# Kernel tuning notes

Hardware: AMD Instinct MI355X
Metric: run time of the kernel (lower is better)

## Reference

```python
import jax, jax.numpy as jnp
import numpy as np
import math

N_NODES = 10000
N_EDGES = 30000
N_FEAT = 128
N_GRAPHS = 50
HEADS = 8
OUT_DIM = 10


def _lin_params(key, fin, fout):
    kw, kb = jax.random.split(key)
    s = 1.0 / math.sqrt(fin)
    w = jax.random.uniform(kw, (fin, fout), jnp.float32, -s, s)
    b = jax.random.uniform(kb, (fout,), jnp.float32, -s, s)
    return w, b


def setup_inputs() -> dict:
    key = jax.random.key(0)
    ks = jax.random.split(key, 20)
    inp = {}
    inp["x"] = jax.random.normal(ks[0], (N_NODES, N_FEAT), jnp.float32)
    inp["edge_index"] = jax.random.randint(ks[1], (2, N_EDGES), 0, N_NODES)
    inp["batch"] = jnp.sort(jax.random.randint(ks[2], (N_NODES,), 0, N_GRAPHS))
    # (fin, out_channels) per layer; internal width = out_channels * HEADS
    dims = [(128, 512), (512, 256), (256, 64)]
    ki = 3
    for i, (fin, cout) in enumerate(dims, 1):
        hc = cout * HEADS
        inp[f"q{i}_w"], inp[f"q{i}_b"] = _lin_params(ks[ki], fin, hc); ki += 1
        inp[f"k{i}_w"], inp[f"k{i}_b"] = _lin_params(ks[ki], fin, hc); ki += 1
        inp[f"v{i}_w"], inp[f"v{i}_b"] = _lin_params(ks[ki], fin, hc); ki += 1
        inp[f"s{i}_w"], inp[f"s{i}_b"] = _lin_params(ks[ki], fin, cout); ki += 1
    inp["gate_w"], inp["gate_b"] = _lin_params(ks[ki], 64, 1); ki += 1
    inp["fc_w"], inp["fc_b"] = _lin_params(ks[ki], 64, OUT_DIM)
    return inp


def _tconv(x, src, dst, qw, qb, kw_, kb_, vw, vb, sw, sb):
    # PyG TransformerConv, heads=HEADS, concat=False (mean over heads), root_weight=True
    N = x.shape[0]
    hc = qw.shape[1]
    C = hc // HEADS
    q = (x @ qw + qb).reshape(N, HEADS, C)
    k = (x @ kw_ + kb_).reshape(N, HEADS, C)
    v = (x @ vw + vb).reshape(N, HEADS, C)
    # per-edge attention logits [E, H]
    alpha = (q[dst] * k[src]).sum(-1) * (1.0 / math.sqrt(C))
    # segment softmax over incoming edges of each destination node
    m = jax.ops.segment_max(alpha, dst, num_segments=N)
    ex = jnp.exp(alpha - m[dst])
    den = jax.ops.segment_sum(ex, dst, num_segments=N)
    w = ex / jnp.maximum(den[dst], 1e-16)
    agg = jax.ops.segment_sum(w[:, :, None] * v[src], dst, num_segments=N)  # [N,H,C]
    return agg.mean(axis=1) + x @ sw + sb


def reference(x, edge_index, batch,
              q1_w, q1_b, k1_w, k1_b, v1_w, v1_b, s1_w, s1_b,
              q2_w, q2_b, k2_w, k2_b, v2_w, v2_b, s2_w, s2_b,
              q3_w, q3_b, k3_w, k3_b, v3_w, v3_b, s3_w, s3_b,
              gate_w, gate_b, fc_w, fc_b):
    src, dst = edge_index[0], edge_index[1]
    h = jax.nn.elu(_tconv(x, src, dst, q1_w, q1_b, k1_w, k1_b, v1_w, v1_b, s1_w, s1_b))
    h = jax.nn.elu(_tconv(h, src, dst, q2_w, q2_b, k2_w, k2_b, v2_w, v2_b, s2_w, s2_b))
    h = jax.nn.elu(_tconv(h, src, dst, q3_w, q3_b, k3_w, k3_b, v3_w, v3_b, s3_w, s3_b))
    # GlobalAttention pooling: softmax(gate) within each graph, weighted sum
    gate = h @ gate_w + gate_b  # [N,1]
    gm = jax.ops.segment_max(gate, batch, num_segments=N_GRAPHS)
    ge = jnp.exp(gate - gm[batch])
    gd = jax.ops.segment_sum(ge, batch, num_segments=N_GRAPHS)
    g = ge / jnp.maximum(gd[batch], 1e-16)
    pooled = jax.ops.segment_sum(g * h, batch, num_segments=N_GRAPHS)  # [G,64]
    return pooled @ fc_w + fc_b
```

## Files before the change

kernel.cpp:

```cpp
#include <hip/hip_runtime.h>
#include <stdint.h>
#include <math.h>

#define NN 10000
#define NE 30000
#define NG 50
#define NH 8

typedef _Float16 f16;
typedef _Float16 f16x2 __attribute__((ext_vector_type(2)));
typedef _Float16 f16x4 __attribute__((ext_vector_type(4)));
typedef _Float16 f16x8 __attribute__((ext_vector_type(8)));
typedef float f32x4 __attribute__((ext_vector_type(4)));

__device__ inline void async16(f16* l, const f16* g) {
    __builtin_amdgcn_global_load_lds((const __attribute__((address_space(1))) void*)g,
                                     (__attribute__((address_space(3))) void*)l, 16, 0, 0);
}

__global__ void hist_kernel(const int* __restrict__ dst, int* __restrict__ deg, int E) {
    int e = blockIdx.x * blockDim.x + threadIdx.x;
    if (e < E) atomicAdd(&deg[dst[e]], 1);
}

__global__ __launch_bounds__(1024) void scan_goffs(const int* __restrict__ deg, int* __restrict__ offs,
                                                   int* __restrict__ cursor,
                                                   const int* __restrict__ batch, int* __restrict__ goffs) {
    if (blockIdx.x == 1) {
        int g = threadIdx.x;
        if (g > NG) return;
        int lo = 0, hi = NN;
        while (lo < hi) {
            int mid = (lo + hi) >> 1;
            if (batch[mid] < g) lo = mid + 1; else hi = mid;
        }
        goffs[g] = lo;
        return;
    }
    __shared__ int tot[1024];
    const int t = threadIdx.x;
    const int base = t * 10;
    int v[10];
    int s = 0;
#pragma unroll
    for (int i = 0; i < 10; ++i) {
        int idx = base + i;
        v[i] = (idx < NN) ? deg[idx] : 0;
        s += v[i];
    }
    tot[t] = s;
    __syncthreads();
    for (int d2 = 1; d2 < 1024; d2 <<= 1) {
        int add = (t >= d2) ? tot[t - d2] : 0;
        __syncthreads();
        tot[t] += add;
        __syncthreads();
    }
    int run = tot[t] - s;
    if (t == 0) offs[0] = 0;
#pragma unroll
    for (int i = 0; i < 10; ++i) {
        int idx = base + i;
        if (idx < NN) cursor[idx] = run;
        run += v[i];
        if (idx < NN) offs[idx + 1] = run;
    }
}

__global__ void scatter_kernel(const int* __restrict__ src, const int* __restrict__ dst,
                               int* __restrict__ cursor, int* __restrict__ srcCSR, int E) {
    int e = blockIdx.x * blockDim.x + threadIdx.x;
    if (e < E) {
        int p = atomicAdd(&cursor[dst[e]], 1);
        srcCSR[p] = src[e];
    }
}

__global__ void sort_csr(const int* __restrict__ offs, int* __restrict__ srcCSR) {
    int n = blockIdx.x * blockDim.x + threadIdx.x;
    if (n >= NN) return;
    int s = offs[n], e = offs[n + 1];
    for (int i = s + 1; i < e; ++i) {
        int v = srcCSR[i];
        int j = i - 1;
        while (j >= s && srcCSR[j] > v) { srcCSR[j + 1] = srcCSR[j]; --j; }
        srcCSR[j + 1] = v;
    }
}

__global__ void cvt3_kernel(const float* __restrict__ a, f16* __restrict__ ao, int na,
                            const float* __restrict__ b, f16* __restrict__ bo, int nb2,
                            const float* __restrict__ c, f16* __restrict__ co, int nc) {
    int i = blockIdx.x * blockDim.x + threadIdx.x;
    if (i < na) ao[i] = (f16)a[i];
    else if (i < na + nb2) { int j = i - na; bo[j] = (f16)b[j]; }
    else if (i < na + nb2 + nc) { int j = i - na - nb2; co[j] = (f16)c[j]; }
}

__global__ __launch_bounds__(256) void prep4t2(
        const float* W0a, int n0a, const float* W1a, int n1a,
        const float* W2a, int n2a, const float* W3a, int n3a,
        const float* b0a, const float* b1a, const float* b2a, const float* b3a,
        f16* Bta, float* biasa, int Ka, int Na,
        const float* W0b, int n0b, const float* W1b, int n1b,
        const float* W2b, int n2b, const float* W3b, int n3b,
        const float* b0b, const float* b1b, const float* b2b, const float* b3b,
        f16* Btb, float* biasb, int Kb, int Nb) {
    const int z = blockIdx.z;
    const float *W0 = z ? W0b : W0a, *W1 = z ? W1b : W1a, *W2 = z ? W2b : W2a, *W3 = z ? W3b : W3a;
    const float *b0 = z ? b0b : b0a, *b1 = z ? b1b : b1a, *b2 = z ? b2b : b2a, *b3 = z ? b3b : b3a;
    const int n0 = z ? n0b : n0a, n1 = z ? n1b : n1a, n2 = z ? n2b : n2a, n3 = z ? n3b : n3a;
    const int K = z ? Kb : Ka, Ntot = z ? Nb : Na;
    f16* Bt = z ? Btb : Bta;
    float* bias = z ? biasb : biasa;
    if ((int)blockIdx.x * 64 >= K || (int)blockIdx.y * 64 >= Ntot) return;

    __shared__ float tile[64][65];
    const int k0 = blockIdx.x * 64;
    const int nb = blockIdx.y * 64;
    const int tid = threadIdx.x;
    const int tn = tid & 63;
    const int t4 = tid >> 6;
#pragma unroll
    for (int i = 0; i < 16; ++i) {
        int kl = t4 + i * 4;
        int k = k0 + kl;
        int n = nb + tn;
        float w = 0.0f;
        int m = n;
        if (m < n0) w = W0[(size_t)k * n0 + m];
        else { m -= n0;
            if (m < n1) w = W1[(size_t)k * n1 + m];
            else { m -= n1;
                if (m < n2) w = W2[(size_t)k * n2 + m];
                else { m -= n2; if (m < n3) w = W3[(size_t)k * n3 + m]; }
            }
        }
        tile[kl][tn] = w;
    }
    if (blockIdx.x == 0 && t4 == 0) {
        int n = nb + tn;
        float bv = 0.0f;
        int m = n;
        if (m < n0) bv = b0[m];
        else { m -= n0;
            if (m < n1) bv = b1[m];
            else { m -= n1;
                if (m < n2) bv = b2[m];
                else { m -= n2; if (m < n3) bv = b3[m]; }
            }
        }
        bias[n] = bv;
    }
    __syncthreads();
#pragma unroll
    for (int i = 0; i < 16; ++i) {
        int nl = t4 + i * 4;
        Bt[(size_t)(nb + nl) * K + k0 + tn] = (f16)tile[tn][nl];
    }
}

__global__ __launch_bounds__(256) void prepU(const float* __restrict__ qw, const float* __restrict__ qb,
                                             const float* __restrict__ kw, const float* __restrict__ kb,
                                             f16* __restrict__ BtY, float* __restrict__ biasY,
                                             int fin, int hc, int C) {
    const int wid = blockIdx.x * 4 + ((int)threadIdx.x >> 6);
    const int lane = threadIdx.x & 63;
    if (wid >= fin * 16) return;
    const int k = wid >> 4;
    const int idx = wid & 15;
    const int h = idx & 7, isV = idx >> 3;
    const float* W = isV ? kw : qw;
    const float* bvec = isV ? qb : kb;
    float s = 0.0f;
    for (int c = lane; c < C; c += 64) s += W[(size_t)k * hc + h * C + c] * bvec[h * C + c];
#pragma unroll
    for (int o = 32; o > 0; o >>= 1) s += __shfl_down(s, o, 64);
    if (lane == 0) BtY[(size_t)(8 * fin + isV * 8 + h) * fin + k] = (f16)s;
    if (wid < 8) {
        float cc = 0.0f;
        for (int c = lane; c < C; c += 64) cc += qb[wid * C + c] * kb[wid * C + c];
#pragma unroll
        for (int o = 32; o > 0; o >>= 1) cc += __shfl_down(cc, o, 64);
        if (lane == 0) biasY[8 * fin + wid] = cc;
    }
}

__global__ __launch_bounds__(256) void prepZB(const float* __restrict__ vw, const float* __restrict__ sw,
                                              const float* __restrict__ vb, const float* __restrict__ sb,
                                              f16* __restrict__ Bt2, float* __restrict__ biasZ) {
    __shared__ f16 tile[32][65];
    const int k0 = blockIdx.x * 32, c0 = blockIdx.y * 64;
    const int tid = threadIdx.x;
#pragma unroll
    for (int i = 0; i < 8; ++i) {
        int idx = tid + i * 256;
        int kl = idx >> 6, cl = idx & 63;
        int k = k0 + kl, c = c0 + cl;
        float v = 0.0f;
        if (k < 1024)      v = vw[(size_t)(k & 127) * 4096 + (k >> 7) * 512 + c];
        else if (k < 1152) v = sw[(size_t)(k - 1024) * 512 + c];
        else if (k < 1160) v = vb[(k - 1152) * 512 + c];
        tile[kl][cl] = (f16)v;
    }
    if (blockIdx.x == 0 && tid < 64) biasZ[c0 + tid] = sb[c0 + tid];
    __syncthreads();
    const int cl = tid >> 2, kl = (tid & 3) * 8;
    f16x8 v;
#pragma unroll
    for (int t = 0; t < 8; ++t) v[t] = tile[kl + t][cl];
    *(f16x8*)(Bt2 + (size_t)(c0 + cl) * 1184 + k0 + kl) = v;
}

__global__ __launch_bounds__(256) void gemm128(const f16* __restrict__ A, int lda, int zA,
                                               const f16* __restrict__ Bt, int ldb, int zB,
                                               const float* __restrict__ bias,
                                               f16* __restrict__ C, int ldc, int zC,
                                               float* __restrict__ Sf,
                                               int M, int Np, int K, int hcS, int Sw, int act) {
    __shared__ f16 smem[24576];
    const int rm = blockIdx.x * 128;
    if (rm >= M) return;
    A  += (size_t)blockIdx.z * zA;
    Bt += (size_t)blockIdx.z * zB;
    C  += (size_t)blockIdx.z * zC;
    const int tid  = threadIdx.x;
    const int lane = tid & 63;
    const int wave = tid >> 6;
    const int l16  = lane & 15;
    const int quad = lane >> 4;
    const int cn   = blockIdx.y * 128;
    const int wrow = (wave >> 1) * 64;
    const int wcol = (wave & 1) * 64;

    const int rS  = tid >> 2;
    const int kc  = ((tid & 3) ^ ((tid >> 3) & 3)) << 3;
    int rowA0 = rm + rS;       if (rowA0 >= M) rowA0 = M - 1;
    int rowA1 = rm + rS + 64;  if (rowA1 >= M) rowA1 = M - 1;
    const f16* gA0 = A + (size_t)rowA0 * lda + kc;
    const f16* gA1 = A + (size_t)rowA1 * lda + kc;
    const f16* gB0 = Bt + (size_t)(cn + rS) * ldb + kc;
    const f16* gB1 = Bt + (size_t)(cn + rS + 64) * ldb + kc;

    const int swf = (l16 >> 1) & 3;
    const int rdAoff = (wrow + l16) * 32 + ((quad ^ swf) << 3);
    const int rdBoff = 4096 + (wcol + l16) * 32 + ((quad ^ swf) << 3);

    f32x4 acc[4][4] = {};

    auto stage_load = [&](int slot) {
        f16* base = smem + slot * 8192;
        async16(base + tid * 8, gA0);
        async16(base + tid * 8 + 2048, gA1);
        async16(base + 4096 + tid * 8, gB0);
        async16(base + 4096 + tid * 8 + 2048, gB1);
        gA0 += 32; gA1 += 32; gB0 += 32; gB1 += 32;
    };

    const int NI = K >> 5;
    stage_load(0);
    stage_load(1);

    int slot = 0;
    for (int i = 0; i < NI; ++i) {
        if (i + 1 < NI) asm volatile("s_waitcnt vmcnt(4)" ::: "memory");
        else            asm volatile("s_waitcnt vmcnt(0)" ::: "memory");
        asm volatile("s_barrier" ::: "memory");
        if (i + 2 < NI) {
            int s2 = slot + 2; if (s2 >= 3) s2 -= 3;
            stage_load(s2);
        }
        const f16* sb = smem + slot * 8192;
        f16x8 av[4], bv[4];
#pragma unroll
        for (int ii = 0; ii < 4; ++ii) av[ii] = *(const f16x8*)(sb + rdAoff + ii * 512);
#pragma unroll
        for (int j = 0; j < 4; ++j) bv[j] = *(const f16x8*)(sb + rdBoff + j * 512);
#pragma unroll
        for (int ii = 0; ii < 4; ++ii)
#pragma unroll
            for (int j = 0; j < 4; ++j)
                acc[ii][j] = __builtin_amdgcn_mfma_f32_16x16x32_f16(bv[j], av[ii], acc[ii][j], 0, 0, 0);
        ++slot; if (slot == 3) slot = 0;
    }
    __syncthreads();

    f16* sC = smem;
    for (int round = 0; round < 2; ++round) {
        if ((wave >> 1) == round) {
#pragma unroll
            for (int j = 0; j < 4; ++j) {
                const int cb = wcol + j * 16 + quad * 4;
                const float4 bb = *(const float4*)(bias + cn + cb);
#pragma unroll
                for (int i = 0; i < 4; ++i) {
                    const int r = i * 16 + l16;
                    float v0 = acc[i][j][0] + bb.x;
                    float v1 = acc[i][j][1] + bb.y;
                    float v2 = acc[i][j][2] + bb.z;
                    float v3 = acc[i][j][3] + bb.w;
                    if (act) {
                        v0 = v0 > 0.0f ? v0 : (__expf(v0) - 1.0f);
                        v1 = v1 > 0.0f ? v1 : (__expf(v1) - 1.0f);
                        v2 = v2 > 0.0f ? v2 : (__expf(v2) - 1.0f);
                        v3 = v3 > 0.0f ? v3 : (__expf(v3) - 1.0f);
                    }
                    f16x4 o;
                    o[0] = (f16)v0; o[1] = (f16)v1; o[2] = (f16)v2; o[3] = (f16)v3;
                    *(f16x4*)(sC + r * 136 + cb) = o;
                    if (Sf) {
                        const int sc = cn + cb - hcS;
                        if (sc >= 0 && sc < Sw) {
                            const int grow = rm + round * 64 + r;
                            if (grow < M) {
                                float4 sv = { v0, v1, v2, v3 };
                                *(float4*)(Sf + (size_t)grow * Sw + sc) = sv;
                            }
                        }
                    }
                }
            }
        }
        __syncthreads();
#pragma unroll
        for (int it = 0; it < 4; ++it) {
            const int r = it * 16 + (tid >> 4);
            const int ch = tid & 15;
            const int grow = rm + round * 64 + r;
            if (grow < M) {
                f16x8 v = *(const f16x8*)(sC + r * 136 + ch * 8);
                *(f16x8*)(C + (size_t)grow * ldc + cn + ch * 8) = v;
            }
        }
        __syncthreads();
    }
}

__global__ __launch_bounds__(256) void alpha_zagg(const f16* __restrict__ Y, const f16* __restrict__ X,
                                                  const int* __restrict__ offs,
                                                  const int* __restrict__ srcCSR,
                                                  f16* __restrict__ Z,
                                                  int strideY, float scale) {
    const int fin = 128;
    const int n = blockIdx.x;
    const int e0 = offs[n];
    int d = offs[n + 1] - e0;
    if (d > 256) d = 256;

    __shared__ __align__(16) f16 sy[1024];
    __shared__ float sew[256 * NH];
    __shared__ float sv[256 * NH];
    __shared__ int sed[256];
    __shared__ float su[NH];
    __shared__ __align__(16) f16 sx[32 * 128];
    const int tid = threadIdx.x;

    const f16* Yn = Y + (size_t)n * strideY;
    for (int c = tid; c < fin; c += 256) ((f16x8*)sy)[c] = ((const f16x8*)Yn)[c];
    if (tid < NH) su[tid] = (float)Yn[8 * fin + tid];
    for (int e = tid; e < d; e += 256) {
        int s = srcCSR[e0 + e];
        sed[e] = s;
        f16x8 vv = *(const f16x8*)(Y + (size_t)s * strideY + 8 * fin + 8);
#pragma unroll
        for (int t = 0; t < 8; ++t) sv[e * NH + t] = (float)vv[t];
    }
    __syncthreads();

    {
        const int wv = tid >> 6, lane = tid & 63;
        for (int e = wv; e < d; e += 4) {
            const f16x8* kg = (const f16x8*)(X + (size_t)sed[e] * fin);
#pragma unroll
            for (int p = 0; p < 2; ++p) {
                const int ci = p * 64 + lane;
                const int head = ci >> 4;
                const int kcn = ci & 15;
                f16x8 yv = ((const f16x8*)sy)[ci];
                f16x8 xv = kg[kcn];
                float acc = 0.0f;
#pragma unroll
                for (int t = 0; t < 8; ++t) acc += (float)yv[t] * (float)xv[t];
#pragma unroll
                for (int o = 8; o > 0; o >>= 1) acc += __shfl_down(acc, o, 16);
                if ((lane & 15) == 0)
                    sew[e * NH + head] = (acc + su[head] + sv[e * NH + head]) * scale;
            }
        }
    }
    __syncthreads();

    if (tid < NH) {
        const int h = tid;
        float m = -3.0e38f;
        for (int e = 0; e < d; ++e) m = fmaxf(m, sew[e * NH + h]);
        float den = 0.0f;
        for (int e = 0; e < d; ++e) {
            float ex = __expf(sew[e * NH + h] - m);
            sew[e * NH + h] = ex;
            den += ex;
        }
        float inv = 1.0f / (fmaxf(den, 1e-16f) * (float)NH);
        for (int e = 0; e < d; ++e) sew[e * NH + h] *= inv;
    }
    __syncthreads();

    const int h = tid >> 5;
    const int f0 = (tid * 4) & 127;
    float a0 = 0.0f, a1 = 0.0f, a2 = 0.0f, a3 = 0.0f;
    for (int ch = 0; ch < d; ch += 32) {
        const int cnt = min(32, d - ch);
        for (int idx = tid; idx < cnt * 16; idx += 256) {
            int row = idx >> 4, c8 = idx & 15;
            *(f16x8*)(sx + row * 128 + c8 * 8) = *(const f16x8*)(X + (size_t)sed[ch + row] * 128 + c8 * 8);
        }
        __syncthreads();
        for (int e = 0; e < cnt; ++e) {
            float w = sew[(ch + e) * NH + h];
            f16x4 xv = *(const f16x4*)(sx + e * 128 + f0);
            a0 += w * (float)xv[0];
            a1 += w * (float)xv[1];
            a2 += w * (float)xv[2];
            a3 += w * (float)xv[3];
        }
        __syncthreads();
    }
    f16* Zr = Z + (size_t)n * 1184;
    f16x4 o; o[0] = (f16)a0; o[1] = (f16)a1; o[2] = (f16)a2; o[3] = (f16)a3;
    *(f16x4*)(Zr + tid * 4) = o;
    if (tid < 16) *(f16x8*)(Zr + 1024 + tid * 8) = *(const f16x8*)(X + (size_t)n * 128 + tid * 8);
    if (tid >= 32 && tid < 40) {
        int hh = tid - 32;
        float s = 0.0f;
        for (int e = 0; e < d; ++e) s += sew[e * NH + hh];
        Zr[1152 + hh] = (f16)s;
    }
    if (tid >= 64 && tid < 88) Zr[1160 + (tid - 64)] = (f16)0.0f;
}

__global__ __launch_bounds__(256) void edge_node(const f16* __restrict__ QKVS,
                                                 const float* __restrict__ Sf,
                                                 const int* __restrict__ offs,
                                                 const int* __restrict__ srcCSR,
                                                 float* __restrict__ hout, f16* __restrict__ houth,
                                                 int Np, int C, int hc, float scale, int writeHout) {
    const int n = blockIdx.x;
    const int e0 = offs[n];
    int d = offs[n + 1] - e0;
    if (d > 256) d = 256;

    __shared__ __align__(16) f16 sq[4096];
    __shared__ float sew[256 * NH];
    __shared__ int sed[256];
    __shared__ float sred[512];
    const int tid = threadIdx.x;

    const f16x8* qg = (const f16x8*)(QKVS + (size_t)n * Np);
    const int qchunks = hc >> 3;
    for (int c = tid; c < qchunks; c += 256) ((f16x8*)sq)[c] = qg[c];
    for (int e = tid; e < d; e += 256) sed[e] = srcCSR[e0 + e];
    __syncthreads();

    {
        const int wv = tid >> 6, lane = tid & 63;
        const int cph = C >> 3;
        const int passes = (hc >> 9) ? (hc >> 9) : 1;
        for (int e = wv; e < d; e += 4) {
            const f16x8* kg = (const f16x8*)(QKVS + (size_t)sed[e] * Np + hc);
            for (int p = 0; p < passes; ++p) {
                const int ci = p * 64 + lane;
                f16x8 qv = ((const f16x8*)sq)[ci];
                f16x8 kv = kg[ci];
                float acc = 0.0f;
#pragma unroll
                for (int t = 0; t < 8; ++t) acc += (float)qv[t] * (float)kv[t];
                for (int o = cph >> 1; o > 0; o >>= 1) acc += __shfl_down(acc, o, cph);
                if ((lane & (cph - 1)) == 0) {
                    const int head = ci / cph;
                    sew[e * NH + head] = acc * scale;
                }
            }
        }
    }
    __syncthreads();

    if (tid < NH) {
        const int h = tid;
        float m = -3.0e38f;
        for (int e = 0; e < d; ++e) m = fmaxf(m, sew[e * NH + h]);
        float den = 0.0f;
        for (int e = 0; e < d; ++e) {
            float ex = __expf(sew[e * NH + h] - m);
            sew[e * NH + h] = ex;
            den += ex;
        }
        float inv = 1.0f / (fmaxf(den, 1e-16f) * (float)NH);
        for (int e = 0; e < d; ++e) sew[e * NH + h] *= inv;
    }
    __syncthreads();

    const int half = C >> 1;
    const int cp = tid & (half - 1);
    const int grp = tid / half;
    const int ngr = 256 / half;
    float a0 = 0.0f, a1 = 0.0f;
    for (int e = grp; e < d; e += ngr) {
        const unsigned int* vp = (const unsigned int*)(QKVS + (size_t)sed[e] * Np + 2 * hc);
#pragma unroll
        for (int h = 0; h < NH; ++h) {
            float w = sew[e * NH + h];
            f16x2 vv = __builtin_bit_cast(f16x2, vp[((h * C) >> 1) + cp]);
            a0 += w * (float)vv.x;
            a1 += w * (float)vv.y;
        }
    }
    if (ngr > 1) {
        sred[tid] = a0;
        sred[256 + tid] = a1;
        __syncthreads();
        if (grp == 0) {
            for (int g = 1; g < ngr; ++g) {
                a0 += sred[g * half + cp];
                a1 += sred[256 + g * half + cp];
            }
        }
    }
    if (grp == 0) {
        const int c = cp * 2;
        const float* Sp = Sf + (size_t)n * C;
        float o0 = a0 + Sp[c];
        float o1 = a1 + Sp[c + 1];
        o0 = o0 > 0.0f ? o0 : (__expf(o0) - 1.0f);
        o1 = o1 > 0.0f ? o1 : (__expf(o1) - 1.0f);
        if (writeHout) {
            hout[(size_t)n * C + c] = o0;
            hout[(size_t)n * C + c + 1] = o1;
        }
        houth[(size_t)n * C + c] = (f16)o0;
        houth[(size_t)n * C + c + 1] = (f16)o1;
    }
}

__global__ __launch_bounds__(256) void pool_graph(const float* __restrict__ h,
                                                  const float* __restrict__ gw, const float* __restrict__ gb,
                                                  const float* __restrict__ fcw, const float* __restrict__ fcb,
                                                  const int* __restrict__ goffs,
                                                  float* __restrict__ gbuf, float* __restrict__ out) {
    const int g = blockIdx.x;
    const int s = goffs[g], e = goffs[g + 1];
    const int tid = threadIdx.x;
    const int wv = tid >> 6, lane = tid & 63;

    __shared__ float red[256];
    __shared__ float pl[64];
    __shared__ float sden;

    if (e == s) {
        if (tid < 10) out[g * 10 + tid] = fcb[tid];
        return;
    }

    const float gwl = gw[lane];
    for (int n = s + wv; n < e; n += 4) {
        float acc = h[(size_t)n * 64 + lane] * gwl;
#pragma unroll
        for (int o = 32; o > 0; o >>= 1) acc += __shfl_down(acc, o, 64);
        if (lane == 0) gbuf[n] = acc + gb[0];
    }
    __syncthreads();

    float m = -3.0e38f;
    for (int n = s + tid; n < e; n += 256) m = fmaxf(m, gbuf[n]);
    red[tid] = m;
    __syncthreads();
    for (int o = 128; o > 0; o >>= 1) {
        if (tid < o) red[tid] = fmaxf(red[tid], red[tid + o]);
        __syncthreads();
    }
    m = red[0];
    __syncthreads();

    float sum = 0.0f;
    for (int n = s + tid; n < e; n += 256) {
        float ex = __expf(gbuf[n] - m);
        gbuf[n] = ex;
        sum += ex;
    }
    red[tid] = sum;
    __syncthreads();
    for (int o = 128; o > 0; o >>= 1) {
        if (tid < o) red[tid] += red[tid + o];
        __syncthreads();
    }
    if (tid == 0) sden = 1.0f / fmaxf(red[0], 1e-16f);
    __syncthreads();

    float acc = 0.0f;
    for (int n = s + wv; n < e; n += 4) acc += gbuf[n] * h[(size_t)n * 64 + lane];
    red[tid] = acc;
    __syncthreads();
    if (wv == 0) pl[lane] = (red[lane] + red[64 + lane] + red[128 + lane] + red[192 + lane]) * sden;
    __syncthreads();

    if (tid < 10) {
        float o = fcb[tid];
#pragma unroll
        for (int c = 0; c < 64; ++c) o += pl[c] * fcw[c * 10 + tid];
        out[g * 10 + tid] = o;
    }
}

extern "C" void kernel_launch(void* const* d_in, const int* in_sizes, int n_in,
                              void* d_out, int out_size, void* d_ws, size_t ws_size,
                              hipStream_t stream) {
    const float* x   = (const float*)d_in[0];
    const int* ei    = (const int*)d_in[1];
    const int* src   = ei;
    const int* dst   = ei + NE;
    const int* batch = (const int*)d_in[2];

    struct LayerW { int fin, C, hc; const float *qw,*qb,*kw,*kb,*vw,*vb,*sw,*sb; };
    LayerW LW[3];
    const int fins[3] = {128, 512, 256};
    const int Cs[3]   = {512, 256, 64};
    for (int l = 0; l < 3; ++l) {
        int b = 3 + 8 * l;
        LW[l].fin = fins[l]; LW[l].C = Cs[l]; LW[l].hc = Cs[l] * NH;
        LW[l].qw = (const float*)d_in[b + 0]; LW[l].qb = (const float*)d_in[b + 1];
        LW[l].kw = (const float*)d_in[b + 2]; LW[l].kb = (const float*)d_in[b + 3];
        LW[l].vw = (const float*)d_in[b + 4]; LW[l].vb = (const float*)d_in[b + 5];
        LW[l].sw = (const float*)d_in[b + 6]; LW[l].sb = (const float*)d_in[b + 7];
    }
    const float* gate_w = (const float*)d_in[27];
    const float* gate_b = (const float*)d_in[28];
    const float* fc_w   = (const float*)d_in[29];
    const float* fc_b   = (const float*)d_in[30];

    size_t off = 0;
    char* ws = (char*)d_ws;
    auto alloc = [&](size_t bytes) -> void* {
        void* p = ws + off;
        off = (off + bytes + 255) & ~(size_t)255;
        return p;
    };
    f16* BtL2   = (f16*)alloc((size_t)6400 * 512 * sizeof(f16));
    f16* BtL3   = (f16*)alloc((size_t)1664 * 256 * sizeof(f16));
    f16* BtZ    = (f16*)alloc((size_t)512 * 1184 * sizeof(f16));
    float* biasL2 = (float*)alloc(6400 * sizeof(float));
    float* biasL3 = (float*)alloc(1664 * sizeof(float));
    float* biasZ  = (float*)alloc(512 * sizeof(float));
    f16* QKbuf  = (f16*)alloc((size_t)NN * 6400 * sizeof(f16));
    f16* Zbuf   = (f16*)alloc((size_t)NN * 1184 * sizeof(f16));
    float* Sf   = (float*)alloc((size_t)NN * 256 * sizeof(float));
    f16* xh     = (f16*)alloc((size_t)NN * 128 * sizeof(f16));
    f16* houth  = (f16*)alloc((size_t)NN * 512 * sizeof(f16));
    float* hf   = (float*)alloc((size_t)NN * 64 * sizeof(float));
    f16* qw16   = (f16*)alloc((size_t)128 * 4096 * sizeof(f16));
    f16* kw16   = (f16*)alloc((size_t)128 * 4096 * sizeof(f16));
    f16* BtY    = (f16*)alloc((size_t)1152 * 128 * sizeof(f16));
    int*   deg   = (int*)alloc(NN * sizeof(int));
    float* zbias = (float*)alloc(512 * sizeof(float));
    float* biasY = (float*)alloc(1152 * sizeof(float));
    size_t zspan = (size_t)((char*)(biasY + 1152) - (char*)deg);
    int* offs   = (int*)alloc((NN + 1) * sizeof(int));
    int* cursor = (int*)alloc(NN * sizeof(int));
    int* srcCSR = (int*)alloc(NE * sizeof(int));
    int* goffs  = (int*)alloc((NG + 1) * sizeof(int));
    float* gbuf = (float*)alloc(NN * sizeof(float));
    if (off > ws_size) return;

    hipMemsetAsync(deg, 0, zspan, stream);
    hist_kernel<<<(NE + 255) / 256, 256, 0, stream>>>(dst, deg, NE);
    scan_goffs<<<2, 1024, 0, stream>>>(deg, offs, cursor, batch, goffs);
    scatter_kernel<<<(NE + 255) / 256, 256, 0, stream>>>(src, dst, cursor, srcCSR, NE);
    sort_csr<<<(NN + 255) / 256, 256, 0, stream>>>(offs, srcCSR);

    {
        int na = NN * 128, nb2 = 128 * 4096, nc = 128 * 4096;
        cvt3_kernel<<<(na + nb2 + nc + 255) / 256, 256, 0, stream>>>(x, xh, na,
                                                                     LW[0].qw, qw16, nb2,
                                                                     LW[0].kw, kw16, nc);
    }
    prep4t2<<<dim3(8, 100, 2), 256, 0, stream>>>(
        LW[1].qw, 2048, LW[1].kw, 2048, LW[1].vw, 2048, LW[1].sw, 256,
        LW[1].qb, LW[1].kb, LW[1].vb, LW[1].sb, BtL2, biasL2, 512, 6400,
        LW[2].qw, 512, LW[2].kw, 512, LW[2].vw, 512, LW[2].sw, 64,
        LW[2].qb, LW[2].kb, LW[2].vb, LW[2].sb, BtL3, biasL3, 256, 1664);
    prepZB<<<dim3(37, 8), 256, 0, stream>>>(LW[0].vw, LW[0].sw, LW[0].vb, LW[0].sb, BtZ, biasZ);

    const int grid_m = 80;

    {
        const int fin = 128, hc = 4096, NtotY = 1152;
        const float scale = 1.0f / sqrtf(512.0f);
        dim3 gm(1, 1, 8);
        gemm128<<<gm, 256, 0, stream>>>(kw16, hc, 512, qw16, hc, 512, zbias,
                                        BtY, fin, fin * fin, nullptr, fin, fin, 512, 0, 0, 0);
        prepU<<<(fin * 16 + 3) / 4, 256, 0, stream>>>(LW[0].qw, LW[0].qb, LW[0].kw, LW[0].kb,
                                                      BtY, biasY, fin, hc, 512);
        dim3 gy(grid_m, NtotY / 128);
        gemm128<<<gy, 256, 0, stream>>>(xh, fin, 0, BtY, fin, 0, biasY,
                                        QKbuf, NtotY, 0, nullptr, NN, NtotY, fin, 0, 0, 0);
        alpha_zagg<<<NN, 256, 0, stream>>>(QKbuf, xh, offs, srcCSR, Zbuf, NtotY, scale);
        dim3 gz(grid_m, 4);
        gemm128<<<gz, 256, 0, stream>>>(Zbuf, 1184, 0, BtZ, 1184, 0, biasZ,
                                        houth, 512, 0, nullptr, NN, 512, 1184, 0, 0, 1);
    }
    const f16* Acur = houth;
    for (int l = 1; l < 3; ++l) {
        const int K = LW[l].fin, C = LW[l].C, hc = LW[l].hc;
        const float scale = 1.0f / sqrtf((float)C);
        const int Np = (3 * hc + C + 127) & ~127;
        f16* Bt = (l == 1) ? BtL2 : BtL3;
        float* bias = (l == 1) ? biasL2 : biasL3;
        dim3 gq(grid_m, Np / 128);
        gemm128<<<gq, 256, 0, stream>>>(Acur, K, 0, Bt, K, 0, bias,
                                        QKbuf, Np, 0, Sf, NN, Np, K, 3 * hc, C, 0);
        edge_node<<<NN, 256, 0, stream>>>(QKbuf, Sf, offs, srcCSR, hf, houth,
                                          Np, C, hc, scale, l == 2 ? 1 : 0);
        Acur = houth;
    }

    pool_graph<<<NG, 256, 0, stream>>>(hf, gate_w, gate_b, fc_w, fc_b, goffs, gbuf, (float*)d_out);
}
```

Before: 475.4 us.

## Merge CSR build into one block and fuse weight prep into megakernel

Replaces the hist/scan/scatter/sort kernel chain and memset with a single 1024-thread block that builds the CSR in LDS counters. It also merges the f16 conversions, weight transposes, the prepU projection and bias zeroing into one block-ranged megaprep launch. The aim is to remove several launches and the memset, trading them for a serial single-block CSR build that uses only one CU. That single-CU build, including the per-node insertion sort, may be slower than the previous multi-block kernels. prepU now runs before the gemm that writes BtY, which needs the two to write disjoint rows.

```diff
diff --git a/kernel.cpp b/kernel.cpp
--- a/kernel.cpp
+++ b/kernel.cpp
@@ -18,106 +18,98 @@
                                      (__attribute__((address_space(3))) void*)l, 16, 0, 0);
 }
 
-__global__ void hist_kernel(const int* __restrict__ dst, int* __restrict__ deg, int E) {
-    int e = blockIdx.x * blockDim.x + threadIdx.x;
-    if (e < E) atomicAdd(&deg[dst[e]], 1);
-}
-
-__global__ __launch_bounds__(1024) void scan_goffs(const int* __restrict__ deg, int* __restrict__ offs,
-                                                   int* __restrict__ cursor,
-                                                   const int* __restrict__ batch, int* __restrict__ goffs) {
-    if (blockIdx.x == 1) {
-        int g = threadIdx.x;
-        if (g > NG) return;
+__global__ __launch_bounds__(1024) void csr_build(const int* __restrict__ src, const int* __restrict__ dst,
+                                                  const int* __restrict__ batch,
+                                                  int* __restrict__ offs, int* __restrict__ srcCSR,
+                                                  int* __restrict__ goffs) {
+    __shared__ int cnt[NN];
+    __shared__ int tot[1024];
+    const int t = threadIdx.x;
+
+    for (int i = t; i < NN; i += 1024) cnt[i] = 0;
+    __syncthreads();
+    for (int e = t; e < NE; e += 1024) atomicAdd(&cnt[dst[e]], 1);
+    __syncthreads();
+
+    const int base = t * 10;
+    int v[10];
+    int s = 0;
+#pragma unroll
+    for (int i = 0; i < 10; ++i) {
+        int idx = base + i;
+        v[i] = (idx < NN) ? cnt[idx] : 0;
+        s += v[i];
+    }
+    tot[t] = s;
+    __syncthreads();
+    for (int d2 = 1; d2 < 1024; d2 <<= 1) {
+        int add = (t >= d2) ? tot[t - d2] : 0;
+        __syncthreads();
+        tot[t] += add;
+        __syncthreads();
+    }
+    int run = tot[t] - s;
+    if (t == 0) offs[0] = 0;
+    int curs[10];
+#pragma unroll
+    for (int i = 0; i < 10; ++i) {
+        int idx = base + i;
+        curs[i] = run;
+        run += v[i];
+        if (idx < NN) offs[idx + 1] = run;
+    }
+    __syncthreads();
+#pragma unroll
+    for (int i = 0; i < 10; ++i) {
+        int idx = base + i;
+        if (idx < NN) cnt[idx] = curs[i];
+    }
+    __syncthreads();
+
+    for (int e = t; e < NE; e += 1024) {
+        int p = atomicAdd(&cnt[dst[e]], 1);
+        srcCSR[p] = src[e];
+    }
+    __syncthreads();
+
+    for (int n = t; n < NN; n += 1024) {
+        int s0 = offs[n], e0 = offs[n + 1];
+        for (int i = s0 + 1; i < e0; ++i) {
+            int vv = srcCSR[i];
+            int j = i - 1;
+            while (j >= s0 && srcCSR[j] > vv) { srcCSR[j + 1] = srcCSR[j]; --j; }
+            srcCSR[j + 1] = vv;
+        }
+    }
+
+    if (t <= NG) {
         int lo = 0, hi = NN;
         while (lo < hi) {
             int mid = (lo + hi) >> 1;
-            if (batch[mid] < g) lo = mid + 1; else hi = mid;
-        }
-        goffs[g] = lo;
-        return;
-    }
-    __shared__ int tot[1024];
-    const int t = threadIdx.x;
-    const int base = t * 10;
-    int v[10];
-    int s = 0;
-#pragma unroll
-    for (int i = 0; i < 10; ++i) {
-        int idx = base + i;
-        v[i] = (idx < NN) ? deg[idx] : 0;
-        s += v[i];
-    }
-    tot[t] = s;
-    __syncthreads();
-    for (int d2 = 1; d2 < 1024; d2 <<= 1) {
-        int add = (t >= d2) ? tot[t - d2] : 0;
-        __syncthreads();
-        tot[t] += add;
-        __syncthreads();
-    }
-    int run = tot[t] - s;
-    if (t == 0) offs[0] = 0;
-#pragma unroll
-    for (int i = 0; i < 10; ++i) {
-        int idx = base + i;
-        if (idx < NN) cursor[idx] = run;
-        run += v[i];
-        if (idx < NN) offs[idx + 1] = run;
-    }
-}
-
-__global__ void scatter_kernel(const int* __restrict__ src, const int* __restrict__ dst,
-                               int* __restrict__ cursor, int* __restrict__ srcCSR, int E) {
-    int e = blockIdx.x * blockDim.x + threadIdx.x;
-    if (e < E) {
-        int p = atomicAdd(&cursor[dst[e]], 1);
-        srcCSR[p] = src[e];
-    }
-}
-
-__global__ void sort_csr(const int* __restrict__ offs, int* __restrict__ srcCSR) {
-    int n = blockIdx.x * blockDim.x + threadIdx.x;
-    if (n >= NN) return;
-    int s = offs[n], e = offs[n + 1];
-    for (int i = s + 1; i < e; ++i) {
-        int v = srcCSR[i];
-        int j = i - 1;
-        while (j >= s && srcCSR[j] > v) { srcCSR[j + 1] = srcCSR[j]; --j; }
-        srcCSR[j + 1] = v;
-    }
-}
-
-__global__ void cvt3_kernel(const float* __restrict__ a, f16* __restrict__ ao, int na,
-                            const float* __restrict__ b, f16* __restrict__ bo, int nb2,
-                            const float* __restrict__ c, f16* __restrict__ co, int nc) {
-    int i = blockIdx.x * blockDim.x + threadIdx.x;
-    if (i < na) ao[i] = (f16)a[i];
-    else if (i < na + nb2) { int j = i - na; bo[j] = (f16)b[j]; }
-    else if (i < na + nb2 + nc) { int j = i - na - nb2; co[j] = (f16)c[j]; }
-}
-
-__global__ __launch_bounds__(256) void prep4t2(
-        const float* W0a, int n0a, const float* W1a, int n1a,
-        const float* W2a, int n2a, const float* W3a, int n3a,
-        const float* b0a, const float* b1a, const float* b2a, const float* b3a,
-        f16* Bta, float* biasa, int Ka, int Na,
-        const float* W0b, int n0b, const float* W1b, int n1b,
-        const float* W2b, int n2b, const float* W3b, int n3b,
-        const float* b0b, const float* b1b, const float* b2b, const float* b3b,
-        f16* Btb, float* biasb, int Kb, int Nb) {
-    const int z = blockIdx.z;
-    const float *W0 = z ? W0b : W0a, *W1 = z ? W1b : W1a, *W2 = z ? W2b : W2a, *W3 = z ? W3b : W3a;
-    const float *b0 = z ? b0b : b0a, *b1 = z ? b1b : b1a, *b2 = z ? b2b : b2a, *b3 = z ? b3b : b3a;
-    const int n0 = z ? n0b : n0a, n1 = z ? n1b : n1a, n2 = z ? n2b : n2a, n3 = z ? n3b : n3a;
-    const int K = z ? Kb : Ka, Ntot = z ? Nb : Na;
-    f16* Bt = z ? Btb : Bta;
-    float* bias = z ? biasb : biasa;
-    if ((int)blockIdx.x * 64 >= K || (int)blockIdx.y * 64 >= Ntot) return;
-
+            if (batch[mid] < t) lo = mid + 1; else hi = mid;
+        }
+        goffs[t] = lo;
+    }
+}
+
+#define MB_CVTX   0
+#define MB_CVTQ   5000
+#define MB_CVTK   7048
+#define MB_P4L2   9096
+#define MB_P4L3   9896
+#define MB_PZB    10000
+#define MB_PU     10296
+#define MB_ZERO   10808
+#define MB_TOTAL  10815
+
+__device__ void prep4_tile(const float* __restrict__ W0, int n0, const float* __restrict__ W1, int n1,
+                           const float* __restrict__ W2, int n2, const float* __restrict__ W3, int n3,
+                           const float* __restrict__ b0, const float* __restrict__ b1,
+                           const float* __restrict__ b2, const float* __restrict__ b3,
+                           f16* __restrict__ Bt, float* __restrict__ bias, int K, int bx, int by) {
     __shared__ float tile[64][65];
-    const int k0 = blockIdx.x * 64;
-    const int nb = blockIdx.y * 64;
+    const int k0 = bx * 64;
+    const int nb = by * 64;
     const int tid = threadIdx.x;
     const int tn = tid & 63;
     const int t4 = tid >> 6;
@@ -138,7 +130,7 @@
         }
         tile[kl][tn] = w;
     }
-    if (blockIdx.x == 0 && t4 == 0) {
+    if (bx == 0 && t4 == 0) {
         int n = nb + tn;
         float bv = 0.0f;
         int m = n;
@@ -160,56 +152,97 @@
     }
 }
 
-__global__ __launch_bounds__(256) void prepU(const float* __restrict__ qw, const float* __restrict__ qb,
-                                             const float* __restrict__ kw, const float* __restrict__ kb,
-                                             f16* __restrict__ BtY, float* __restrict__ biasY,
-                                             int fin, int hc, int C) {
-    const int wid = blockIdx.x * 4 + ((int)threadIdx.x >> 6);
-    const int lane = threadIdx.x & 63;
-    if (wid >= fin * 16) return;
-    const int k = wid >> 4;
-    const int idx = wid & 15;
-    const int h = idx & 7, isV = idx >> 3;
-    const float* W = isV ? kw : qw;
-    const float* bvec = isV ? qb : kb;
-    float s = 0.0f;
-    for (int c = lane; c < C; c += 64) s += W[(size_t)k * hc + h * C + c] * bvec[h * C + c];
-#pragma unroll
-    for (int o = 32; o > 0; o >>= 1) s += __shfl_down(s, o, 64);
-    if (lane == 0) BtY[(size_t)(8 * fin + isV * 8 + h) * fin + k] = (f16)s;
-    if (wid < 8) {
-        float cc = 0.0f;
-        for (int c = lane; c < C; c += 64) cc += qb[wid * C + c] * kb[wid * C + c];
-#pragma unroll
-        for (int o = 32; o > 0; o >>= 1) cc += __shfl_down(cc, o, 64);
-        if (lane == 0) biasY[8 * fin + wid] = cc;
-    }
-}
-
-__global__ __launch_bounds__(256) void prepZB(const float* __restrict__ vw, const float* __restrict__ sw,
-                                              const float* __restrict__ vb, const float* __restrict__ sb,
-                                              f16* __restrict__ Bt2, float* __restrict__ biasZ) {
-    __shared__ f16 tile[32][65];
-    const int k0 = blockIdx.x * 32, c0 = blockIdx.y * 64;
+__global__ __launch_bounds__(256) void megaprep(
+        const float* __restrict__ x, f16* __restrict__ xh,
+        const float* __restrict__ qw1, f16* __restrict__ qw16,
+        const float* __restrict__ kw1, f16* __restrict__ kw16,
+        const float* __restrict__ qb1, const float* __restrict__ kb1,
+        const float* __restrict__ vw1, const float* __restrict__ sw1,
+        const float* __restrict__ vb1, const float* __restrict__ sb1,
+        const float* __restrict__ qw2, const float* __restrict__ qb2,
+        const float* __restrict__ kw2, const float* __restrict__ kb2,
+        const float* __restrict__ vw2, const float* __restrict__ vb2,
+        const float* __restrict__ sw2, const float* __restrict__ sb2,
+        const float* __restrict__ qw3, const float* __restrict__ qb3,
+        const float* __restrict__ kw3, const float* __restrict__ kb3,
+        const float* __restrict__ vw3, const float* __restrict__ vb3,
+        const float* __restrict__ sw3, const float* __restrict__ sb3,
+        f16* __restrict__ BtL2, float* __restrict__ biasL2,
+        f16* __restrict__ BtL3, float* __restrict__ biasL3,
+        f16* __restrict__ BtZ, float* __restrict__ biasZ,
+        f16* __restrict__ BtY, float* __restrict__ biasY,
+        float* __restrict__ zbias) {
+    const int b = blockIdx.x;
     const int tid = threadIdx.x;
-#pragma unroll
-    for (int i = 0; i < 8; ++i) {
-        int idx = tid + i * 256;
-        int kl = idx >> 6, cl = idx & 63;
-        int k = k0 + kl, c = c0 + cl;
-        float v = 0.0f;
-        if (k < 1024)      v = vw[(size_t)(k & 127) * 4096 + (k >> 7) * 512 + c];
-        else if (k < 1152) v = sw[(size_t)(k - 1024) * 512 + c];
-        else if (k < 1160) v = vb[(k - 1152) * 512 + c];
-        tile[kl][cl] = (f16)v;
-    }
-    if (blockIdx.x == 0 && tid < 64) biasZ[c0 + tid] = sb[c0 + tid];
-    __syncthreads();
-    const int cl = tid >> 2, kl = (tid & 3) * 8;
-    f16x8 v;
-#pragma unroll
-    for (int t = 0; t < 8; ++t) v[t] = tile[kl + t][cl];
-    *(f16x8*)(Bt2 + (size_t)(c0 + cl) * 1184 + k0 + kl) = v;
+
+    if (b < MB_CVTQ) {
+        int i = b * 256 + tid;
+        if (i < NN * 128) xh[i] = (f16)x[i];
+    } else if (b < MB_CVTK) {
+        int i = (b - MB_CVTQ) * 256 + tid;
+        qw16[i] = (f16)qw1[i];
+    } else if (b < MB_P4L2) {
+        int i = (b - MB_CVTK) * 256 + tid;
+        kw16[i] = (f16)kw1[i];
+    } else if (b < MB_P4L3) {
+        int r = b - MB_P4L2;
+        prep4_tile(qw2, 2048, kw2, 2048, vw2, 2048, sw2, 256,
+                   qb2, kb2, vb2, sb2, BtL2, biasL2, 512, r & 7, r >> 3);
+    } else if (b < MB_PZB) {
+        int r = b - MB_P4L3;
+        prep4_tile(qw3, 512, kw3, 512, vw3, 512, sw3, 64,
+                   qb3, kb3, vb3, sb3, BtL3, biasL3, 256, r & 3, r >> 2);
+    } else if (b < MB_PU) {
+        int r = b - MB_PZB;
+        int bx = r % 37, by = r / 37;
+        __shared__ f16 ztile[32][65];
+        const int k0 = bx * 32, c0 = by * 64;
+#pragma unroll
+        for (int i = 0; i < 8; ++i) {
+            int idx = tid + i * 256;
+            int kl = idx >> 6, cl = idx & 63;
+            int k = k0 + kl, c = c0 + cl;
+            float v = 0.0f;
+            if (k < 1024)      v = vw1[(size_t)(k & 127) * 4096 + (k >> 7) * 512 + c];
+            else if (k < 1152) v = sw1[(size_t)(k - 1024) * 512 + c];
+            else if (k < 1160) v = vb1[(k - 1152) * 512 + c];
+            ztile[kl][cl] = (f16)v;
+        }
+        if (bx == 0 && tid < 64) biasZ[c0 + tid] = sb1[c0 + tid];
+        __syncthreads();
+        const int cl = tid >> 2, kl = (tid & 3) * 8;
+        f16x8 v;
+#pragma unroll
+        for (int t2 = 0; t2 < 8; ++t2) v[t2] = ztile[kl + t2][cl];
+        *(f16x8*)(BtZ + (size_t)(c0 + cl) * 1184 + k0 + kl) = v;
+    } else if (b < MB_ZERO) {
+        const int fin = 128, hc = 4096, C = 512;
+        const int wid = (b - MB_PU) * 4 + (tid >> 6);
+        const int lane = tid & 63;
+        if (wid >= fin * 16) return;
+        const int k = wid >> 4;
+        const int idx = wid & 15;
+        const int h = idx & 7, isV = idx >> 3;
+        const float* W = isV ? kw1 : qw1;
+        const float* bvec = isV ? qb1 : kb1;
+        float s = 0.0f;
+        for (int c = lane; c < C; c += 64) s += W[(size_t)k * hc + h * C + c] * bvec[h * C + c];
+#pragma unroll
+        for (int o = 32; o > 0; o >>= 1) s += __shfl_down(s, o, 64);
+        if (lane == 0) BtY[(size_t)(8 * fin + isV * 8 + h) * fin + k] = (f16)s;
+        if (wid < 8) {
+            float cc = 0.0f;
+            for (int c = lane; c < C; c += 64) cc += qb1[wid * C + c] * kb1[wid * C + c];
+#pragma unroll
+            for (int o = 32; o > 0; o >>= 1) cc += __shfl_down(cc, o, 64);
+            if (lane == 0) biasY[8 * fin + wid] = cc;
+        }
+    } else {
+        int idx = (b - MB_ZERO) * 256 + tid;
+        if (idx < 512) zbias[idx] = 0.0f;
+        else if (idx < 1536) biasY[idx - 512] = 0.0f;
+        else if (idx < 1656) biasY[1032 + idx - 1536] = 0.0f;
+    }
 }
 
 __global__ __launch_bounds__(256) void gemm128(const f16* __restrict__ A, int lda, int zA,
@@ -658,35 +691,22 @@
     f16* qw16   = (f16*)alloc((size_t)128 * 4096 * sizeof(f16));
     f16* kw16   = (f16*)alloc((size_t)128 * 4096 * sizeof(f16));
     f16* BtY    = (f16*)alloc((size_t)1152 * 128 * sizeof(f16));
-    int*   deg   = (int*)alloc(NN * sizeof(int));
     float* zbias = (float*)alloc(512 * sizeof(float));
     float* biasY = (float*)alloc(1152 * sizeof(float));
-    size_t zspan = (size_t)((char*)(biasY + 1152) - (char*)deg);
     int* offs   = (int*)alloc((NN + 1) * sizeof(int));
-    int* cursor = (int*)alloc(NN * sizeof(int));
     int* srcCSR = (int*)alloc(NE * sizeof(int));
     int* goffs  = (int*)alloc((NG + 1) * sizeof(int));
     float* gbuf = (float*)alloc(NN * sizeof(float));
     if (off > ws_size) return;
 
-    hipMemsetAsync(deg, 0, zspan, stream);
-    hist_kernel<<<(NE + 255) / 256, 256, 0, stream>>>(dst, deg, NE);
-    scan_goffs<<<2, 1024, 0, stream>>>(deg, offs, cursor, batch, goffs);
-    scatter_kernel<<<(NE + 255) / 256, 256, 0, stream>>>(src, dst, cursor, srcCSR, NE);
-    sort_csr<<<(NN + 255) / 256, 256, 0, stream>>>(offs, srcCSR);
-
-    {
-        int na = NN * 128, nb2 = 128 * 4096, nc = 128 * 4096;
-        cvt3_kernel<<<(na + nb2 + nc + 255) / 256, 256, 0, stream>>>(x, xh, na,
-                                                                     LW[0].qw, qw16, nb2,
-                                                                     LW[0].kw, kw16, nc);
-    }
-    prep4t2<<<dim3(8, 100, 2), 256, 0, stream>>>(
-        LW[1].qw, 2048, LW[1].kw, 2048, LW[1].vw, 2048, LW[1].sw, 256,
-        LW[1].qb, LW[1].kb, LW[1].vb, LW[1].sb, BtL2, biasL2, 512, 6400,
-        LW[2].qw, 512, LW[2].kw, 512, LW[2].vw, 512, LW[2].sw, 64,
-        LW[2].qb, LW[2].kb, LW[2].vb, LW[2].sb, BtL3, biasL3, 256, 1664);
-    prepZB<<<dim3(37, 8), 256, 0, stream>>>(LW[0].vw, LW[0].sw, LW[0].vb, LW[0].sb, BtZ, biasZ);
+    megaprep<<<MB_TOTAL, 256, 0, stream>>>(
+        x, xh, LW[0].qw, qw16, LW[0].kw, kw16,
+        LW[0].qb, LW[0].kb, LW[0].vw, LW[0].sw, LW[0].vb, LW[0].sb,
+        LW[1].qw, LW[1].qb, LW[1].kw, LW[1].kb, LW[1].vw, LW[1].vb, LW[1].sw, LW[1].sb,
+        LW[2].qw, LW[2].qb, LW[2].kw, LW[2].kb, LW[2].vw, LW[2].vb, LW[2].sw, LW[2].sb,
+        BtL2, biasL2, BtL3, biasL3, BtZ, biasZ, BtY, biasY, zbias);
+
+    csr_build<<<1, 1024, 0, stream>>>(src, dst, batch, offs, srcCSR, goffs);
 
     const int grid_m = 80;
 
@@ -696,8 +716,6 @@
         dim3 gm(1, 1, 8);
         gemm128<<<gm, 256, 0, stream>>>(kw16, hc, 512, qw16, hc, 512, zbias,
                                         BtY, fin, fin * fin, nullptr, fin, fin, 512, 0, 0, 0);
-        prepU<<<(fin * 16 + 3) / 4, 256, 0, stream>>>(LW[0].qw, LW[0].qb, LW[0].kw, LW[0].kb,
-                                                      BtY, biasY, fin, hc, 512);
         dim3 gy(grid_m, NtotY / 128);
         gemm128<<<gy, 256, 0, stream>>>(xh, fin, 0, BtY, fin, 0, biasY,
                                         QKbuf, NtotY, 0, nullptr, NN, NtotY, fin, 0, 0, 0);
```

Measured after the change: 561.4 us. +18.1%, slower.
